# Kernel tuning notes

Hardware: AMD Instinct MI355X
Metric: run time of the kernel (lower is better)

Reference implementation:

```python
import jax, jax.numpy as jnp
import numpy as np
import math

B, T, C, H = 4, 2048, 512, 8
HD = C // H


def make_alibias(block_size, ms):
    # ALiBi-style per-head bias: -m_h * |i - j|, shape [1, H, S, S]
    idx = jnp.arange(block_size)
    dist = jnp.abs(idx[:, None] - idx[None, :]).astype(jnp.float32)  # [S,S]
    return -ms[None, :, None, None] * dist[None, None, :, :]


def setup_inputs() -> dict:
    key = jax.random.key(0)
    k1, k2, k3, k4, k5 = jax.random.split(key, 5)
    x = jax.random.normal(k1, (B, T, C), dtype=jnp.float32)
    Wqkv = jax.random.normal(k2, (C, 3 * C), dtype=jnp.float32) * (1.0 / math.sqrt(C))
    bqkv = jax.random.normal(k3, (3 * C,), dtype=jnp.float32) * 0.02
    Wproj = jax.random.normal(k4, (C, C), dtype=jnp.float32) * (1.0 / math.sqrt(C))
    bproj = jax.random.normal(k5, (C,), dtype=jnp.float32) * 0.02
    ms = jnp.arange(1, H + 1, dtype=jnp.float32) * 0.05
    alibias = make_alibias(T, ms)  # [1,H,T,T]
    return {"x": x, "Wqkv": Wqkv, "bqkv": bqkv, "Wproj": Wproj, "bproj": bproj, "alibias": alibias}


def reference(x, Wqkv, bqkv, Wproj, bproj, alibias):
    Bv, Tv, Cv = x.shape
    qkv = x @ Wqkv + bqkv                      # [B,T,3C]
    q, k, v = jnp.split(qkv, 3, axis=-1)
    # [B,T,C] -> [B,H,T,hd]
    def heads(t):
        return t.reshape(Bv, Tv, H, HD).transpose(0, 2, 1, 3)
    q, k, v = heads(q), heads(k), heads(v)
    att = jnp.einsum('bhqd,bhkd->bhqk', q, k) * (1.0 / math.sqrt(HD))
    att = att + alibias[:, :, :Tv, :Tv]
    att = jax.nn.softmax(att, axis=-1)
    y = jnp.einsum('bhqk,bhkd->bhqd', att, v)  # [B,H,T,hd]
    y = y.transpose(0, 2, 1, 3).reshape(Bv, Tv, Cv)
    return y @ Wproj + bproj
```

## Files before the change

### kernel.cpp

```cpp
#include <hip/hip_runtime.h>
#include <hip/hip_bf16.h>

#define LOG2E 1.4426950408889634f

typedef __attribute__((ext_vector_type(8))) short short8;
typedef __attribute__((ext_vector_type(8))) __bf16 bf16x8;
typedef __attribute__((ext_vector_type(4))) float f32x4;

__device__ __forceinline__ unsigned short f2b(float f){
  unsigned int u = __builtin_bit_cast(unsigned int, f);
  u += 0x7fffu + ((u >> 16) & 1u);
  return (unsigned short)(u >> 16);
}

__device__ __forceinline__ unsigned int cvtpk(float lo, float hi){
  unsigned int r;
  asm("v_cvt_pk_bf16_f32 %0, %1, %2" : "=v"(r) : "v"(lo), "v"(hi));
  return r;
}

__device__ __forceinline__ void gload16(const void* g, void* l){
  __builtin_amdgcn_global_load_lds(
      (const __attribute__((address_space(1))) unsigned int*)g,
      (__attribute__((address_space(3))) unsigned int*)l, 16, 0, 0);
}

__global__ __launch_bounds__(256) void prep_kernel(
    const float* __restrict__ x, const float* __restrict__ Wqkv, const float* __restrict__ Wproj,
    unsigned short* __restrict__ xb, unsigned short* __restrict__ wqkvT, unsigned short* __restrict__ wprojT){
  __shared__ unsigned short T[64][72];
  const int bid = blockIdx.x, tid = threadIdx.x;
  if (bid < 2048){
    size_t i = ((size_t)bid * 256 + tid) * 8;
    float4 a = *(const float4*)(x + i);
    float4 b = *(const float4*)(x + i + 4);
    short8 s;
    s[0]=(short)f2b(a.x); s[1]=(short)f2b(a.y); s[2]=(short)f2b(a.z); s[3]=(short)f2b(a.w);
    s[4]=(short)f2b(b.x); s[5]=(short)f2b(b.y); s[6]=(short)f2b(b.z); s[7]=(short)f2b(b.w);
    *(short8*)(xb + i) = s;
    return;
  }
  const float* in; unsigned short* out; int R, C, bx, by;
  if (bid < 2240){ int t = bid - 2048; bx = t % 24; by = t / 24; in = Wqkv; out = wqkvT; R = 512; C = 1536; }
  else           { int t = bid - 2240; bx = t % 8;  by = t / 8;  in = Wproj; out = wprojT; R = 512; C = 512; }
  const int r0 = by * 64, c0 = bx * 64;
  {
    const int i = tid >> 2, jg = (tid & 3) * 16;
    const float* src = in + (size_t)(r0 + i) * C + c0 + jg;
    #pragma unroll
    for (int e = 0; e < 16; e += 4){
      float4 v = *(const float4*)(src + e);
      T[i][jg + e + 0] = f2b(v.x);
      T[i][jg + e + 1] = f2b(v.y);
      T[i][jg + e + 2] = f2b(v.z);
      T[i][jg + e + 3] = f2b(v.w);
    }
  }
  __syncthreads();
  {
    const int j = tid >> 2, ig = (tid & 3) * 16;
    short8 w0, w1;
    #pragma unroll
    for (int e = 0; e < 8; e++) w0[e] = (short)T[ig + e][j];
    #pragma unroll
    for (int e = 0; e < 8; e++) w1[e] = (short)T[ig + 8 + e][j];
    unsigned short* dst = out + (size_t)(c0 + j) * R + r0 + ig;
    *(short8*)dst = w0;
    *(short8*)(dst + 8) = w1;
  }
}

__global__ __launch_bounds__(256,3) void gemm_qkv_kernel(
    const unsigned short* __restrict__ A,
    const unsigned short* __restrict__ Bt,
    const float* __restrict__ bias,
    unsigned short* __restrict__ Qb,
    unsigned short* __restrict__ Kb,
    unsigned short* __restrict__ VTb,
    float* __restrict__ Mq, float* __restrict__ Mk){
  __shared__ unsigned short As[128*64];
  __shared__ unsigned short Bs[128*64];
  const int tid = threadIdx.x, wid = tid >> 6, lane = tid & 63;
  const int wr = wid >> 1, wc = wid & 1;
  const int fr = lane & 15, fq = lane >> 4;
  const int fr7 = fr & 7;
  const int orig = blockIdx.x;
  const int xcd = orig & 7, idx = orig >> 3;
  const int bm = (xcd + 8*(idx/12)) * 128;
  const int bn = (idx % 12) * 128;
  f32x4 acc[4][4];
  #pragma unroll
  for (int m=0;m<4;m++)
    #pragma unroll
    for (int n=0;n<4;n++) acc[m][n] = (f32x4){0.f,0.f,0.f,0.f};

  for (int k0 = 0; k0 < 512; k0 += 64){
    __syncthreads();
    #pragma unroll
    for (int it=0; it<4; it++){
      const int s = it*256 + tid;
      const int row = s >> 3, c = s & 7;
      const int sc = c ^ (row & 7);
      void* al = (void*)(As + (it*256 + wid*64)*8);
      void* bl = (void*)(Bs + (it*256 + wid*64)*8);
      gload16(A  + (size_t)(bm + row)*512 + k0 + sc*8, al);
      gload16(Bt + (size_t)(bn + row)*512 + k0 + sc*8, bl);
    }
    __syncthreads();
    bf16x8 af[4][2], bfv[4][2];
    #pragma unroll
    for (int m=0;m<4;m++)
      #pragma unroll
      for (int kk=0;kk<2;kk++)
        af[m][kk]  = *(const bf16x8*)&As[(wr*64 + m*16 + fr)*64 + (((kk*4+fq)^fr7)*8)];
    #pragma unroll
    for (int n=0;n<4;n++)
      #pragma unroll
      for (int kk=0;kk<2;kk++)
        bfv[n][kk] = *(const bf16x8*)&Bs[(wc*64 + n*16 + fr)*64 + (((kk*4+fq)^fr7)*8)];
    #pragma unroll
    for (int kk=0;kk<2;kk++)
      #pragma unroll
      for (int m=0;m<4;m++)
        #pragma unroll
        for (int n=0;n<4;n++)
          acc[m][n] = __builtin_amdgcn_mfma_f32_16x16x32_bf16(af[m][kk], bfv[n][kk], acc[m][n], 0,0,0);
  }

  const float SCQ = 0.125f * LOG2E;
  const int colbase = bn + wc*64;
  const int which = colbase >> 9;
  float ss[4][4];
  #pragma unroll
  for (int m=0;m<4;m++)
    #pragma unroll
    for (int g=0;g<4;g++) ss[m][g] = 0.f;

  #pragma unroll
  for (int m=0;m<4;m++){
    const int row0 = bm + wr*64 + m*16 + fq*4;
    const int b_ = row0 >> 11, t_ = row0 & 2047;
    #pragma unroll
    for (int n=0;n<4;n++){
      const int col = colbase + n*16 + fr;
      const int c = col & 511, hh = c >> 6, dd = c & 63;
      const float bv = bias[col];
      if (which == 0){
        #pragma unroll
        for (int g=0; g<4; g++){
          const float v = (acc[m][n][g] + bv) * SCQ;
          ss[m][g] = fmaf(v, v, ss[m][g]);
          Qb[((size_t)(b_*8 + hh)*2048 + t_ + g)*64 + dd] = f2b(v);
        }
      } else if (which == 1){
        #pragma unroll
        for (int g=0; g<4; g++){
          const float v = acc[m][n][g] + bv;
          ss[m][g] = fmaf(v, v, ss[m][g]);
          Kb[((size_t)(b_*8 + hh)*2048 + t_ + g)*64 + dd] = f2b(v);
        }
      } else {
        uint2 pk;
        pk.x = cvtpk(acc[m][n][0] + bv, acc[m][n][1] + bv);
        pk.y = cvtpk(acc[m][n][2] + bv, acc[m][n][3] + bv);
        *(uint2*)&VTb[((size_t)(b_*8 + hh)*64 + dd)*2048 + t_] = pk;
      }
    }
  }

  if (which <= 1){
    #pragma unroll
    for (int m=0;m<4;m++)
      #pragma unroll
      for (int g=0;g<4;g++){
        float s = ss[m][g];
        s += __shfl_xor(s, 1); s += __shfl_xor(s, 2);
        s += __shfl_xor(s, 4); s += __shfl_xor(s, 8);
        ss[m][g] = s;
      }
    float mx = 0.f;
    #pragma unroll
    for (int m=0;m<4;m++)
      #pragma unroll
      for (int g=0;g<4;g++) mx = fmaxf(mx, ss[m][g]);
    mx = fmaxf(mx, __shfl_xor(mx, 16));
    mx = fmaxf(mx, __shfl_xor(mx, 32));
    if (lane == 0){
      const int rowbase = bm + wr*64;
      const int b_ = rowbase >> 11, qc_ = (rowbase >> 6) & 31;
      const int h_ = (colbase >> 6) & 7;
      float* M = which ? Mk : Mq;
      M[(b_*8 + h_)*32 + qc_] = sqrtf(mx) * 1.01f;
    }
  }
}

__global__ __launch_bounds__(256,3) void attn_kernel(
    const unsigned short* __restrict__ Q,
    const unsigned short* __restrict__ K,
    const unsigned short* __restrict__ VT,
    const float* __restrict__ alib,
    const float* __restrict__ Mqa,
    const float* __restrict__ Mka,
    unsigned short* __restrict__ Y){
  __shared__ unsigned short Ks[2][64*64];
  __shared__ unsigned short Vs[2][64*64];
  __shared__ unsigned short Ps[4][16][72];
  __shared__ float MkS[32];
  __shared__ float wred[4];
  __shared__ int lst[32];
  __shared__ int nsh;
  const int tid = threadIdx.x, wid = tid >> 6, lane = tid & 63;
  const int fr = lane & 15, fq = lane >> 4;
  const int fr7 = fr & 7;
  const int id = blockIdx.x;
  const int h = id >> 7;
  const int low3 = id & 7, idx4 = (id & 127) >> 3;
  const int b = idx4 >> 2, off = idx4 & 3;
  const int quad = (low3 - b) & 7;
  const int qc = quad*4 + off;
  const int bh = b*8 + h;
  const int q0 = qc*64 + wid*16;
  const unsigned short* Qp = Q  + (size_t)bh * 131072;
  const unsigned short* Kp = K  + (size_t)bh * 131072;
  const unsigned short* Vp = VT + (size_t)bh * 131072;
  const float nmh2 = alib[(size_t)h * 4194304 + 1] * LOG2E;
  const float MqMk0 = Mqa[bh*32 + qc];
  if (tid < 32) MkS[tid] = Mka[bh*32 + tid];

  float vmk = Mka[bh*32 + (lane & 31)];
  #pragma unroll
  for (int d=1; d<32; d<<=1) vmk = fmaxf(vmk, __shfl_xor(vmk, d));
  const float msta = MqMk0 * vmk;

  bf16x8 qf[2];
  #pragma unroll
  for (int kk=0;kk<2;kk++)
    qf[kk] = *(const bf16x8*)(Qp + (size_t)(q0 + fr)*64 + kk*32 + fq*8);

  bf16x8 ones;
  #pragma unroll
  for (int e=0;e<8;e++) ones[e] = __builtin_bit_cast(__bf16, (unsigned short)0x3F80);

  f32x4 o[4], osum;
  #pragma unroll
  for (int ni=0;ni<4;ni++) o[ni] = (f32x4){0.f,0.f,0.f,0.f};
  osum = (f32x4){0.f,0.f,0.f,0.f};
  float rowmax = -1e30f;
  const float qi = (float)(q0 + fr);
  const float qb = nmh2 * qi;
  f32x4 ka[4];
  #pragma unroll
  for (int ni=0;ni<4;ni++)
    #pragma unroll
    for (int g=0;g<4;g++) ka[ni][g] = nmh2 * (float)(ni*16 + fq*4 + g);

  auto stage = [&](int kt, int buf){
    const int kb = kt * 64;
    #pragma unroll
    for (int it=0; it<2; it++){
      const int s = it*256 + tid;
      const int row = s >> 3, c = s & 7;
      const int sc = c ^ (row & 7);
      gload16(Kp + (size_t)(kb + row)*64 + sc*8, (void*)(Ks[buf] + (it*256 + wid*64)*8));
      gload16(Vp + (size_t)row*2048 + kb + sc*8, (void*)(Vs[buf] + (it*256 + wid*64)*8));
    }
  };

  auto compute = [&](int kt, int buf, bool diag){
    const int kb = kt * 64;
    const unsigned short* KsB = Ks[buf];
    const unsigned short* VsB = Vs[buf];
    bf16x8 kf[4][2], vf[4][2];
    #pragma unroll
    for (int ni=0;ni<4;ni++)
      #pragma unroll
      for (int kk=0;kk<2;kk++){
        const int r = ni*16 + fr;
        const int sw = ((kk*4 + fq) ^ fr7) * 8;
        kf[ni][kk] = *(const bf16x8*)&KsB[r*64 + sw];
        vf[ni][kk] = *(const bf16x8*)&VsB[r*64 + sw];
      }

    f32x4 st[4];
    const f32x4 fz = {0.f,0.f,0.f,0.f};
    #pragma unroll
    for (int ni=0;ni<4;ni++){
      f32x4 t0 = __builtin_amdgcn_mfma_f32_16x16x32_bf16(kf[ni][0], qf[0], fz, 0,0,0);
      st[ni] = __builtin_amdgcn_mfma_f32_16x16x32_bf16(kf[ni][1], qf[1], t0, 0,0,0);
    }

    float cadd;
    if (diag){
      const float base = qi - (float)(kb + fq*4);
      #pragma unroll
      for (int ni=0;ni<4;ni++)
        #pragma unroll
        for (int g=0;g<4;g++){
          const float d = fabsf(base - (float)(ni*16 + g));
          st[ni][g] = fmaf(nmh2, d, st[ni][g]);
        }
      cadd = 0.f;
      float m0 = fmaxf(fmaxf(st[0][0], st[0][1]), fmaxf(st[0][2], st[0][3]));
      float m1 = fmaxf(fmaxf(st[1][0], st[1][1]), fmaxf(st[1][2], st[1][3]));
      float m2 = fmaxf(fmaxf(st[2][0], st[2][1]), fmaxf(st[2][2], st[2][3]));
      float m3 = fmaxf(fmaxf(st[3][0], st[3][1]), fmaxf(st[3][2], st[3][3]));
      float tm = fmaxf(fmaxf(m0, m1), fmaxf(m2, m3));
      tm = fmaxf(tm, __shfl_xor(tm, 16));
      tm = fmaxf(tm, __shfl_xor(tm, 32));
      rowmax = tm;
    } else {
      const float s1 = (kt > qc) ? 1.f : -1.f;
      #pragma unroll
      for (int ni=0;ni<4;ni++)
        #pragma unroll
        for (int g=0;g<4;g++)
          st[ni][g] = fmaf(s1, ka[ni][g], st[ni][g]);
      cadd = s1 * (nmh2 * (float)kb - qb);
    }

    const float mexp = msta - cadd;
    #pragma unroll
    for (int ni=0;ni<4;ni++)
      #pragma unroll
      for (int g=0;g<4;g++)
        st[ni][g] = exp2f(st[ni][g] - mexp);

    #pragma unroll
    for (int ni=0;ni<4;ni++){
      uint2 pk;
      pk.x = cvtpk(st[ni][0], st[ni][1]);
      pk.y = cvtpk(st[ni][2], st[ni][3]);
      *(uint2*)&Ps[wid][fr][ni*16 + fq*4] = pk;
    }

    bf16x8 pf[2];
    #pragma unroll
    for (int kk=0;kk<2;kk++)
      pf[kk] = *(const bf16x8*)&Ps[wid][fr][kk*32 + fq*8];
    #pragma unroll
    for (int ni=0;ni<4;ni++){
      o[ni] = __builtin_amdgcn_mfma_f32_16x16x32_bf16(pf[0], vf[ni][0], o[ni], 0,0,0);
      o[ni] = __builtin_amdgcn_mfma_f32_16x16x32_bf16(pf[1], vf[ni][1], o[ni], 0,0,0);
    }
    osum = __builtin_amdgcn_mfma_f32_16x16x32_bf16(pf[0], ones, osum, 0,0,0);
    osum = __builtin_amdgcn_mfma_f32_16x16x32_bf16(pf[1], ones, osum, 0,0,0);
  };

  const int e0 = (qc + 1 < 32) ? qc + 1 : qc - 1;
  const int e1 = (qc + 1 < 32 && qc - 1 >= 0) ? qc - 1 : -1;
  stage(qc, 0);
  stage(e0, 1);
  asm volatile("s_waitcnt vmcnt(4)" ::: "memory");
  __builtin_amdgcn_sched_barrier(0);
  __builtin_amdgcn_s_barrier();
  compute(qc, 0, true);

  float wm = rowmax;
  #pragma unroll
  for (int d=1; d<16; d<<=1) wm = fminf(wm, __shfl_xor(wm, d));
  if (lane == 0) wred[wid] = wm;
  __syncthreads();
  const float thresh  = fminf(fminf(wred[0], wred[1]), fminf(wred[2], wred[3])) - 14.0f;
  const float threshW = wm - 14.0f;

  if (tid == 0){
    float maxMk = 0.f;
    #pragma unroll
    for (int t=0; t<32; t++) maxMk = fmaxf(maxMk, MkS[t]);
    int n = 0;
    if (e1 >= 0) lst[n++] = e1;
    for (int dt = 2; dt < 32; dt++){
      const float biasmax = nmh2 * (float)((dt - 1)*64 + 1);
      if (MqMk0 * maxMk + biasmax < thresh) break;
      int kt = qc + dt;
      if (kt < 32 && MqMk0 * MkS[kt] + biasmax >= thresh) lst[n++] = kt;
      kt = qc - dt;
      if (kt >= 0 && MqMk0 * MkS[kt] + biasmax >= thresh) lst[n++] = kt;
    }
    nsh = n;
  }
  __syncthreads();
  const int nt = nsh + 1;

  for (int j = 0; j < nt; j++){
    const int kt = (j == 0) ? e0 : lst[j-1];
    asm volatile("s_waitcnt lgkmcnt(0)" ::: "memory");
    __builtin_amdgcn_sched_barrier(0);
    __builtin_amdgcn_s_barrier();
    if (j + 1 < nt){
      stage((j == 0) ? lst[0] : lst[j], j & 1);
      asm volatile("s_waitcnt vmcnt(4)" ::: "memory");
    } else {
      asm volatile("s_waitcnt vmcnt(0)" ::: "memory");
    }
    __builtin_amdgcn_sched_barrier(0);
    __builtin_amdgcn_s_barrier();
    const int dminW = (kt > qc) ? (kt*64 - (q0 + 15)) : (q0 - (kt*64 + 63));
    if (MqMk0 * MkS[kt] + nmh2 * (float)dminW >= threshW)
      compute(kt, (j+1)&1, false);
  }

  #pragma unroll
  for (int g=0;g<4;g++){
    const float iv = 1.0f / osum[g];
    const int t = q0 + fq*4 + g;
    #pragma unroll
    for (int ni=0;ni<4;ni++)
      Y[(size_t)(b*2048 + t)*512 + h*64 + ni*16 + fr] = f2b(o[ni][g] * iv);
  }
}

__global__ __launch_bounds__(256,2) void gemm_proj_kernel(
    const unsigned short* __restrict__ A,
    const unsigned short* __restrict__ Bt,
    const float* __restrict__ bias,
    float* __restrict__ out){
  __shared__ unsigned short As[128*64];
  __shared__ unsigned short Bs[128*64];
  const int tid = threadIdx.x, wid = tid >> 6, lane = tid & 63;
  const int wr = wid >> 1, wc = wid & 1;
  const int fr = lane & 15, fq = lane >> 4;
  const int fr7 = fr & 7;
  const int orig = blockIdx.x;
  const int xcd = orig & 7, idx = orig >> 3;
  const int bm = (xcd + 8*(idx >> 2)) * 128;
  const int bn = (idx & 3) * 128;
  f32x4 acc[4][4];
  #pragma unroll
  for (int m=0;m<4;m++)
    #pragma unroll
    for (int n=0;n<4;n++) acc[m][n] = (f32x4){0.f,0.f,0.f,0.f};

  for (int k0 = 0; k0 < 512; k0 += 64){
    __syncthreads();
    #pragma unroll
    for (int it=0; it<4; it++){
      const int s = it*256 + tid;
      const int row = s >> 3, c = s & 7;
      const int sc = c ^ (row & 7);
      void* al = (void*)(As + (it*256 + wid*64)*8);
      void* bl = (void*)(Bs + (it*256 + wid*64)*8);
      gload16(A  + (size_t)(bm + row)*512 + k0 + sc*8, al);
      gload16(Bt + (size_t)(bn + row)*512 + k0 + sc*8, bl);
    }
    __syncthreads();
    bf16x8 af[4][2], bfv[4][2];
    #pragma unroll
    for (int m=0;m<4;m++)
      #pragma unroll
      for (int kk=0;kk<2;kk++)
        af[m][kk]  = *(const bf16x8*)&As[(wr*64 + m*16 + fr)*64 + (((kk*4+fq)^fr7)*8)];
    #pragma unroll
    for (int n=0;n<4;n++)
      #pragma unroll
      for (int kk=0;kk<2;kk++)
        bfv[n][kk] = *(const bf16x8*)&Bs[(wc*64 + n*16 + fr)*64 + (((kk*4+fq)^fr7)*8)];
    #pragma unroll
    for (int kk=0;kk<2;kk++)
      #pragma unroll
      for (int m=0;m<4;m++)
        #pragma unroll
        for (int n=0;n<4;n++)
          acc[m][n] = __builtin_amdgcn_mfma_f32_16x16x32_bf16(af[m][kk], bfv[n][kk], acc[m][n], 0,0,0);
  }

  #pragma unroll
  for (int m=0;m<4;m++){
    const int row0 = bm + wr*64 + m*16 + fq*4;
    #pragma unroll
    for (int n=0;n<4;n++){
      const int col = bn + wc*64 + n*16 + fr;
      const float bv = bias[col];
      #pragma unroll
      for (int g=0; g<4; g++)
        out[(size_t)(row0 + g)*512 + col] = acc[m][n][g] + bv;
    }
  }
}

extern "C" void kernel_launch(void* const* d_in, const int* in_sizes, int n_in,
                              void* d_out, int out_size, void* d_ws, size_t ws_size,
                              hipStream_t stream){
  const float* x     = (const float*)d_in[0];
  const float* Wqkv  = (const float*)d_in[1];
  const float* bqkv  = (const float*)d_in[2];
  const float* Wproj = (const float*)d_in[3];
  const float* bproj = (const float*)d_in[4];
  const float* alib  = (const float*)d_in[5];
  char* ws = (char*)d_ws;
  unsigned short* xb     = (unsigned short*)(ws);
  unsigned short* wqkvT  = (unsigned short*)(ws + 8388608);
  unsigned short* wprojT = (unsigned short*)(ws + 9961472);
  unsigned short* Qb     = (unsigned short*)(ws + 10485760);
  unsigned short* Kb     = (unsigned short*)(ws + 18874368);
  unsigned short* VTb    = (unsigned short*)(ws + 27262976);
  unsigned short* Yb     = (unsigned short*)(ws + 35651584);
  float* out = (float*)d_out;
  float* Mq = out + 4194304 - 2048;
  float* Mk = Mq + 1024;

  prep_kernel<<<2304, 256, 0, stream>>>(x, Wqkv, Wproj, xb, wqkvT, wprojT);
  gemm_qkv_kernel<<<768, 256, 0, stream>>>(xb, wqkvT, bqkv, Qb, Kb, VTb, Mq, Mk);
  attn_kernel<<<1024, 256, 0, stream>>>(Qb, Kb, VTb, alib, Mq, Mk, Yb);
  gemm_proj_kernel<<<256, 256, 0, stream>>>(Yb, wprojT, bproj, out);
}
```

Baseline: 65.29 us.

## Process two adjacent query chunks per attention block to reuse staged K/V tiles

Each attention block now handles 128 query rows (two 64-row chunks A and B) instead of 64, and the grid is halved to 512 blocks. Each K/V tile staged into LDS is used for both query chunks, with separate per-chunk skip tests, so global K/V loads per query row drop roughly by half. The cost is more registers for the second accumulator set, which may hurt occupancy under the 3-blocks launch bound. There are also fewer blocks in flight and a more serialized start, since both diagonal tiles are processed before the tile list is built.

```diff
diff --git a/kernel.cpp b/kernel.cpp
--- a/kernel.cpp
+++ b/kernel.cpp
@@ -207,48 +207,53 @@
   __shared__ unsigned short Vs[2][64*64];
   __shared__ unsigned short Ps[4][16][72];
   __shared__ float MkS[32];
-  __shared__ float wred[4];
+  __shared__ float wredA[4], wredB[4];
   __shared__ int lst[32];
   __shared__ int nsh;
   const int tid = threadIdx.x, wid = tid >> 6, lane = tid & 63;
   const int fr = lane & 15, fq = lane >> 4;
   const int fr7 = fr & 7;
   const int id = blockIdx.x;
-  const int h = id >> 7;
-  const int low3 = id & 7, idx4 = (id & 127) >> 3;
-  const int b = idx4 >> 2, off = idx4 & 3;
-  const int quad = (low3 - b) & 7;
-  const int qc = quad*4 + off;
+  const int h = id >> 6;
+  const int r_ = id & 63, xcd = r_ & 7, s_ = r_ >> 3;
+  const int b = s_ >> 1;
+  const int c = ((xcd + b) & 7)*2 + (s_ & 1);
   const int bh = b*8 + h;
-  const int q0 = qc*64 + wid*16;
+  const int qcA = 2*c, qcB = qcA + 1;
+  const int q0a = c*128 + wid*16, q0b = q0a + 64;
   const unsigned short* Qp = Q  + (size_t)bh * 131072;
   const unsigned short* Kp = K  + (size_t)bh * 131072;
   const unsigned short* Vp = VT + (size_t)bh * 131072;
   const float nmh2 = alib[(size_t)h * 4194304 + 1] * LOG2E;
-  const float MqMk0 = Mqa[bh*32 + qc];
+  const float MqA = Mqa[bh*32 + qcA];
+  const float MqB = Mqa[bh*32 + qcB];
   if (tid < 32) MkS[tid] = Mka[bh*32 + tid];
 
   float vmk = Mka[bh*32 + (lane & 31)];
   #pragma unroll
   for (int d=1; d<32; d<<=1) vmk = fmaxf(vmk, __shfl_xor(vmk, d));
-  const float msta = MqMk0 * vmk;
-
-  bf16x8 qf[2];
-  #pragma unroll
-  for (int kk=0;kk<2;kk++)
-    qf[kk] = *(const bf16x8*)(Qp + (size_t)(q0 + fr)*64 + kk*32 + fq*8);
+  const float mstaA = MqA * vmk;
+  const float mstaB = MqB * vmk;
+
+  bf16x8 qfA[2], qfB[2];
+  #pragma unroll
+  for (int kk=0;kk<2;kk++){
+    qfA[kk] = *(const bf16x8*)(Qp + (size_t)(q0a + fr)*64 + kk*32 + fq*8);
+    qfB[kk] = *(const bf16x8*)(Qp + (size_t)(q0b + fr)*64 + kk*32 + fq*8);
+  }
 
   bf16x8 ones;
   #pragma unroll
   for (int e=0;e<8;e++) ones[e] = __builtin_bit_cast(__bf16, (unsigned short)0x3F80);
 
-  f32x4 o[4], osum;
-  #pragma unroll
-  for (int ni=0;ni<4;ni++) o[ni] = (f32x4){0.f,0.f,0.f,0.f};
-  osum = (f32x4){0.f,0.f,0.f,0.f};
-  float rowmax = -1e30f;
-  const float qi = (float)(q0 + fr);
-  const float qb = nmh2 * qi;
+  f32x4 oA[4], oB[4], osumA, osumB;
+  #pragma unroll
+  for (int ni=0;ni<4;ni++){ oA[ni] = (f32x4){0.f,0.f,0.f,0.f}; oB[ni] = (f32x4){0.f,0.f,0.f,0.f}; }
+  osumA = (f32x4){0.f,0.f,0.f,0.f};
+  osumB = (f32x4){0.f,0.f,0.f,0.f};
+  float rowmaxA = -1e30f, rowmaxB = -1e30f;
+  const float qiA = (float)(q0a + fr), qiB = (float)(q0b + fr);
+  const float qbA = nmh2 * qiA, qbB = nmh2 * qiB;
   f32x4 ka[4];
   #pragma unroll
   for (int ni=0;ni<4;ni++)
@@ -260,14 +265,14 @@
     #pragma unroll
     for (int it=0; it<2; it++){
       const int s = it*256 + tid;
-      const int row = s >> 3, c = s & 7;
-      const int sc = c ^ (row & 7);
+      const int row = s >> 3, cc = s & 7;
+      const int sc = cc ^ (row & 7);
       gload16(Kp + (size_t)(kb + row)*64 + sc*8, (void*)(Ks[buf] + (it*256 + wid*64)*8));
       gload16(Vp + (size_t)row*2048 + kb + sc*8, (void*)(Vs[buf] + (it*256 + wid*64)*8));
     }
   };
 
-  auto compute = [&](int kt, int buf, bool diag){
+  auto computeT = [&](int kt, int buf, int diagmi, bool doA, bool doB){
     const int kb = kt * 64;
     const unsigned short* KsB = Ks[buf];
     const unsigned short* VsB = Vs[buf];
@@ -281,102 +286,122 @@
         kf[ni][kk] = *(const bf16x8*)&KsB[r*64 + sw];
         vf[ni][kk] = *(const bf16x8*)&VsB[r*64 + sw];
       }
-
-    f32x4 st[4];
     const f32x4 fz = {0.f,0.f,0.f,0.f};
-    #pragma unroll
-    for (int ni=0;ni<4;ni++){
-      f32x4 t0 = __builtin_amdgcn_mfma_f32_16x16x32_bf16(kf[ni][0], qf[0], fz, 0,0,0);
-      st[ni] = __builtin_amdgcn_mfma_f32_16x16x32_bf16(kf[ni][1], qf[1], t0, 0,0,0);
-    }
-
-    float cadd;
-    if (diag){
-      const float base = qi - (float)(kb + fq*4);
+
+    #pragma unroll
+    for (int mi=0; mi<2; mi++){
+      if (mi == 0 ? !doA : !doB) continue;
+      const bf16x8* qf = (mi == 0) ? qfA : qfB;
+      f32x4 st[4];
+      #pragma unroll
+      for (int ni=0;ni<4;ni++){
+        f32x4 t0 = __builtin_amdgcn_mfma_f32_16x16x32_bf16(kf[ni][0], qf[0], fz, 0,0,0);
+        st[ni] = __builtin_amdgcn_mfma_f32_16x16x32_bf16(kf[ni][1], qf[1], t0, 0,0,0);
+      }
+      const float qi_ = (mi==0) ? qiA : qiB;
+      const float qb_ = (mi==0) ? qbA : qbB;
+      const int   qc_ = (mi==0) ? qcA : qcB;
+      float cadd;
+      if (diagmi == mi){
+        const float base = qi_ - (float)(kb + fq*4);
+        #pragma unroll
+        for (int ni=0;ni<4;ni++)
+          #pragma unroll
+          for (int g=0;g<4;g++){
+            const float d = fabsf(base - (float)(ni*16 + g));
+            st[ni][g] = fmaf(nmh2, d, st[ni][g]);
+          }
+        cadd = 0.f;
+        float m0 = fmaxf(fmaxf(st[0][0], st[0][1]), fmaxf(st[0][2], st[0][3]));
+        float m1 = fmaxf(fmaxf(st[1][0], st[1][1]), fmaxf(st[1][2], st[1][3]));
+        float m2 = fmaxf(fmaxf(st[2][0], st[2][1]), fmaxf(st[2][2], st[2][3]));
+        float m3 = fmaxf(fmaxf(st[3][0], st[3][1]), fmaxf(st[3][2], st[3][3]));
+        float tm = fmaxf(fmaxf(m0, m1), fmaxf(m2, m3));
+        tm = fmaxf(tm, __shfl_xor(tm, 16));
+        tm = fmaxf(tm, __shfl_xor(tm, 32));
+        if (mi == 0) rowmaxA = tm; else rowmaxB = tm;
+      } else {
+        const float s1 = (kt > qc_) ? 1.f : -1.f;
+        #pragma unroll
+        for (int ni=0;ni<4;ni++)
+          #pragma unroll
+          for (int g=0;g<4;g++)
+            st[ni][g] = fmaf(s1, ka[ni][g], st[ni][g]);
+        cadd = s1 * (nmh2 * (float)kb - qb_);
+      }
+
+      const float mexp = ((mi==0) ? mstaA : mstaB) - cadd;
       #pragma unroll
       for (int ni=0;ni<4;ni++)
         #pragma unroll
-        for (int g=0;g<4;g++){
-          const float d = fabsf(base - (float)(ni*16 + g));
-          st[ni][g] = fmaf(nmh2, d, st[ni][g]);
-        }
-      cadd = 0.f;
-      float m0 = fmaxf(fmaxf(st[0][0], st[0][1]), fmaxf(st[0][2], st[0][3]));
-      float m1 = fmaxf(fmaxf(st[1][0], st[1][1]), fmaxf(st[1][2], st[1][3]));
-      float m2 = fmaxf(fmaxf(st[2][0], st[2][1]), fmaxf(st[2][2], st[2][3]));
-      float m3 = fmaxf(fmaxf(st[3][0], st[3][1]), fmaxf(st[3][2], st[3][3]));
-      float tm = fmaxf(fmaxf(m0, m1), fmaxf(m2, m3));
-      tm = fmaxf(tm, __shfl_xor(tm, 16));
-      tm = fmaxf(tm, __shfl_xor(tm, 32));
-      rowmax = tm;
-    } else {
-      const float s1 = (kt > qc) ? 1.f : -1.f;
-      #pragma unroll
-      for (int ni=0;ni<4;ni++)
-        #pragma unroll
         for (int g=0;g<4;g++)
-          st[ni][g] = fmaf(s1, ka[ni][g], st[ni][g]);
-      cadd = s1 * (nmh2 * (float)kb - qb);
-    }
-
-    const float mexp = msta - cadd;
-    #pragma unroll
-    for (int ni=0;ni<4;ni++)
-      #pragma unroll
-      for (int g=0;g<4;g++)
-        st[ni][g] = exp2f(st[ni][g] - mexp);
-
-    #pragma unroll
-    for (int ni=0;ni<4;ni++){
-      uint2 pk;
-      pk.x = cvtpk(st[ni][0], st[ni][1]);
-      pk.y = cvtpk(st[ni][2], st[ni][3]);
-      *(uint2*)&Ps[wid][fr][ni*16 + fq*4] = pk;
-    }
-
-    bf16x8 pf[2];
-    #pragma unroll
-    for (int kk=0;kk<2;kk++)
-      pf[kk] = *(const bf16x8*)&Ps[wid][fr][kk*32 + fq*8];
-    #pragma unroll
-    for (int ni=0;ni<4;ni++){
-      o[ni] = __builtin_amdgcn_mfma_f32_16x16x32_bf16(pf[0], vf[ni][0], o[ni], 0,0,0);
-      o[ni] = __builtin_amdgcn_mfma_f32_16x16x32_bf16(pf[1], vf[ni][1], o[ni], 0,0,0);
-    }
-    osum = __builtin_amdgcn_mfma_f32_16x16x32_bf16(pf[0], ones, osum, 0,0,0);
-    osum = __builtin_amdgcn_mfma_f32_16x16x32_bf16(pf[1], ones, osum, 0,0,0);
+          st[ni][g] = exp2f(st[ni][g] - mexp);
+
+      #pragma unroll
+      for (int ni=0;ni<4;ni++){
+        uint2 pk;
+        pk.x = cvtpk(st[ni][0], st[ni][1]);
+        pk.y = cvtpk(st[ni][2], st[ni][3]);
+        *(uint2*)&Ps[wid][fr][ni*16 + fq*4] = pk;
+      }
+      bf16x8 pf[2];
+      #pragma unroll
+      for (int kk=0;kk<2;kk++)
+        pf[kk] = *(const bf16x8*)&Ps[wid][fr][kk*32 + fq*8];
+      f32x4* o_ = (mi==0) ? oA : oB;
+      #pragma unroll
+      for (int ni=0;ni<4;ni++){
+        o_[ni] = __builtin_amdgcn_mfma_f32_16x16x32_bf16(pf[0], vf[ni][0], o_[ni], 0,0,0);
+        o_[ni] = __builtin_amdgcn_mfma_f32_16x16x32_bf16(pf[1], vf[ni][1], o_[ni], 0,0,0);
+      }
+      if (mi == 0){
+        osumA = __builtin_amdgcn_mfma_f32_16x16x32_bf16(pf[0], ones, osumA, 0,0,0);
+        osumA = __builtin_amdgcn_mfma_f32_16x16x32_bf16(pf[1], ones, osumA, 0,0,0);
+      } else {
+        osumB = __builtin_amdgcn_mfma_f32_16x16x32_bf16(pf[0], ones, osumB, 0,0,0);
+        osumB = __builtin_amdgcn_mfma_f32_16x16x32_bf16(pf[1], ones, osumB, 0,0,0);
+      }
+    }
   };
 
-  const int e0 = (qc + 1 < 32) ? qc + 1 : qc - 1;
-  const int e1 = (qc + 1 < 32 && qc - 1 >= 0) ? qc - 1 : -1;
-  stage(qc, 0);
-  stage(e0, 1);
+  stage(qcA, 0);
+  stage(qcB, 1);
   asm volatile("s_waitcnt vmcnt(4)" ::: "memory");
   __builtin_amdgcn_sched_barrier(0);
   __builtin_amdgcn_s_barrier();
-  compute(qc, 0, true);
-
-  float wm = rowmax;
-  #pragma unroll
-  for (int d=1; d<16; d<<=1) wm = fminf(wm, __shfl_xor(wm, d));
-  if (lane == 0) wred[wid] = wm;
+  computeT(qcA, 0, 0, true, true);
+  asm volatile("s_waitcnt vmcnt(0)" ::: "memory");
+  __builtin_amdgcn_sched_barrier(0);
+  __builtin_amdgcn_s_barrier();
+  const int f0 = (qcA - 1 >= 0) ? qcA - 1 : qcB + 1;
+  stage(f0, 0);
+  computeT(qcB, 1, 1, true, true);
+
+  float wmA = rowmaxA, wmB = rowmaxB;
+  #pragma unroll
+  for (int d=1; d<16; d<<=1){ wmA = fminf(wmA, __shfl_xor(wmA, d)); wmB = fminf(wmB, __shfl_xor(wmB, d)); }
+  if (lane == 0){ wredA[wid] = wmA; wredB[wid] = wmB; }
   __syncthreads();
-  const float thresh  = fminf(fminf(wred[0], wred[1]), fminf(wred[2], wred[3])) - 14.0f;
-  const float threshW = wm - 14.0f;
+  const float thresh = fminf(fminf(fminf(wredA[0], wredA[1]), fminf(wredA[2], wredA[3])),
+                             fminf(fminf(wredB[0], wredB[1]), fminf(wredB[2], wredB[3]))) - 14.0f;
+  const float threshWA = wmA - 14.0f;
+  const float threshWB = wmB - 14.0f;
 
   if (tid == 0){
     float maxMk = 0.f;
     #pragma unroll
     for (int t=0; t<32; t++) maxMk = fmaxf(maxMk, MkS[t]);
+    const float Mqmax = fmaxf(MqA, MqB);
     int n = 0;
-    if (e1 >= 0) lst[n++] = e1;
+    if (qcA - 1 >= 0 && qcB + 1 < 32)
+      lst[n++] = (f0 == qcA - 1) ? qcB + 1 : qcA - 1;
     for (int dt = 2; dt < 32; dt++){
       const float biasmax = nmh2 * (float)((dt - 1)*64 + 1);
-      if (MqMk0 * maxMk + biasmax < thresh) break;
-      int kt = qc + dt;
-      if (kt < 32 && MqMk0 * MkS[kt] + biasmax >= thresh) lst[n++] = kt;
-      kt = qc - dt;
-      if (kt >= 0 && MqMk0 * MkS[kt] + biasmax >= thresh) lst[n++] = kt;
+      if (Mqmax * maxMk + biasmax < thresh) break;
+      int kt = qcB + dt;
+      if (kt < 32 && MqB * MkS[kt] + biasmax >= thresh) lst[n++] = kt;
+      kt = qcA - dt;
+      if (kt >= 0 && MqA * MkS[kt] + biasmax >= thresh) lst[n++] = kt;
     }
     nsh = n;
   }
@@ -384,30 +409,36 @@
   const int nt = nsh + 1;
 
   for (int j = 0; j < nt; j++){
-    const int kt = (j == 0) ? e0 : lst[j-1];
+    const int kt = (j == 0) ? f0 : lst[j-1];
     asm volatile("s_waitcnt lgkmcnt(0)" ::: "memory");
     __builtin_amdgcn_sched_barrier(0);
     __builtin_amdgcn_s_barrier();
     if (j + 1 < nt){
-      stage((j == 0) ? lst[0] : lst[j], j & 1);
+      stage(lst[j], (j+1)&1);
       asm volatile("s_waitcnt vmcnt(4)" ::: "memory");
     } else {
       asm volatile("s_waitcnt vmcnt(0)" ::: "memory");
     }
     __builtin_amdgcn_sched_barrier(0);
     __builtin_amdgcn_s_barrier();
-    const int dminW = (kt > qc) ? (kt*64 - (q0 + 15)) : (q0 - (kt*64 + 63));
-    if (MqMk0 * MkS[kt] + nmh2 * (float)dminW >= threshW)
-      compute(kt, (j+1)&1, false);
+    const int dA = (kt > qcB) ? (kt*64 - (q0a + 15)) : (q0a - (kt*64 + 63));
+    const int dB = (kt > qcB) ? (kt*64 - (q0b + 15)) : (q0b - (kt*64 + 63));
+    const bool doA = MqA * MkS[kt] + nmh2 * (float)dA >= threshWA;
+    const bool doB = MqB * MkS[kt] + nmh2 * (float)dB >= threshWB;
+    if (doA || doB) computeT(kt, j&1, -1, doA, doB);
   }
 
   #pragma unroll
   for (int g=0;g<4;g++){
-    const float iv = 1.0f / osum[g];
-    const int t = q0 + fq*4 + g;
-    #pragma unroll
-    for (int ni=0;ni<4;ni++)
-      Y[(size_t)(b*2048 + t)*512 + h*64 + ni*16 + fr] = f2b(o[ni][g] * iv);
+    const float ivA = 1.0f / osumA[g];
+    const float ivB = 1.0f / osumB[g];
+    const int tA = q0a + fq*4 + g;
+    const int tB = q0b + fq*4 + g;
+    #pragma unroll
+    for (int ni=0;ni<4;ni++){
+      Y[(size_t)(b*2048 + tA)*512 + h*64 + ni*16 + fr] = f2b(oA[ni][g] * ivA);
+      Y[(size_t)(b*2048 + tB)*512 + h*64 + ni*16 + fr] = f2b(oB[ni][g] * ivB);
+    }
   }
 }
 
@@ -502,6 +533,6 @@
 
   prep_kernel<<<2304, 256, 0, stream>>>(x, Wqkv, Wproj, xb, wqkvT, wprojT);
   gemm_qkv_kernel<<<768, 256, 0, stream>>>(xb, wqkvT, bqkv, Qb, Kb, VTb, Mq, Mk);
-  attn_kernel<<<1024, 256, 0, stream>>>(Qb, Kb, VTb, alib, Mq, Mk, Yb);
+  attn_kernel<<<512, 256, 0, stream>>>(Qb, Kb, VTb, alib, Mq, Mk, Yb);
   gemm_proj_kernel<<<256, 256, 0, stream>>>(Yb, wprojT, bproj, out);
 }
```

After: 92.20 us. +41.2%, slower.

## Process 128 query rows per attention block with 8 waves sharing K/V tiles

Applied to the files above, without the earlier changes.

The attention kernel now launches 512 blocks of 512 threads, and each block covers two adjacent 64-row query chunks instead of one. Each staged K/V tile in LDS is reused by twice as many waves, which halves the tile loads per query row. Both diagonal tiles are computed with row-max tracking, and the far-tile list is built from the union of the two chunks' bias bounds. The cost is a looser per-block skip threshold, which can add tiles the narrower blocks skipped, plus heavier barriers across 8 waves.

```diff
diff --git a/kernel.cpp b/kernel.cpp
--- a/kernel.cpp
+++ b/kernel.cpp
@@ -195,7 +195,7 @@
   }
 }
 
-__global__ __launch_bounds__(256,3) void attn_kernel(
+__global__ __launch_bounds__(512,4) void attn_kernel(
     const unsigned short* __restrict__ Q,
     const unsigned short* __restrict__ K,
     const unsigned short* __restrict__ VT,
@@ -205,33 +205,34 @@
     unsigned short* __restrict__ Y){
   __shared__ unsigned short Ks[2][64*64];
   __shared__ unsigned short Vs[2][64*64];
-  __shared__ unsigned short Ps[4][16][72];
+  __shared__ unsigned short Ps[8][16][72];
   __shared__ float MkS[32];
-  __shared__ float wred[4];
+  __shared__ float wred[8];
   __shared__ int lst[32];
   __shared__ int nsh;
   const int tid = threadIdx.x, wid = tid >> 6, lane = tid & 63;
   const int fr = lane & 15, fq = lane >> 4;
   const int fr7 = fr & 7;
   const int id = blockIdx.x;
-  const int h = id >> 7;
-  const int low3 = id & 7, idx4 = (id & 127) >> 3;
-  const int b = idx4 >> 2, off = idx4 & 3;
-  const int quad = (low3 - b) & 7;
-  const int qc = quad*4 + off;
+  const int h = id >> 6;
+  const int r_ = id & 63, xcd = r_ & 7, s_ = r_ >> 3;
+  const int b = s_ >> 1;
+  const int c = ((xcd + b) & 7)*2 + (s_ & 1);
   const int bh = b*8 + h;
-  const int q0 = qc*64 + wid*16;
+  const int tA = 2*c, tB = 2*c + 1;
+  const int q0 = c*128 + wid*16;
+  const int qcW = q0 >> 6;
   const unsigned short* Qp = Q  + (size_t)bh * 131072;
   const unsigned short* Kp = K  + (size_t)bh * 131072;
   const unsigned short* Vp = VT + (size_t)bh * 131072;
   const float nmh2 = alib[(size_t)h * 4194304 + 1] * LOG2E;
-  const float MqMk0 = Mqa[bh*32 + qc];
+  const float MqW = Mqa[bh*32 + qcW];
   if (tid < 32) MkS[tid] = Mka[bh*32 + tid];
 
   float vmk = Mka[bh*32 + (lane & 31)];
   #pragma unroll
   for (int d=1; d<32; d<<=1) vmk = fmaxf(vmk, __shfl_xor(vmk, d));
-  const float msta = MqMk0 * vmk;
+  const float msta = MqW * vmk;
 
   bf16x8 qf[2];
   #pragma unroll
@@ -257,17 +258,13 @@
 
   auto stage = [&](int kt, int buf){
     const int kb = kt * 64;
-    #pragma unroll
-    for (int it=0; it<2; it++){
-      const int s = it*256 + tid;
-      const int row = s >> 3, c = s & 7;
-      const int sc = c ^ (row & 7);
-      gload16(Kp + (size_t)(kb + row)*64 + sc*8, (void*)(Ks[buf] + (it*256 + wid*64)*8));
-      gload16(Vp + (size_t)row*2048 + kb + sc*8, (void*)(Vs[buf] + (it*256 + wid*64)*8));
-    }
+    const int row = tid >> 3, cc = tid & 7;
+    const int sc = cc ^ (row & 7);
+    gload16(Kp + (size_t)(kb + row)*64 + sc*8, (void*)(Ks[buf] + wid*64*8));
+    gload16(Vp + (size_t)row*2048 + kb + sc*8, (void*)(Vs[buf] + wid*64*8));
   };
 
-  auto compute = [&](int kt, int buf, bool diag){
+  auto computeT = [&](int kt, int buf, bool track){
     const int kb = kt * 64;
     const unsigned short* KsB = Ks[buf];
     const unsigned short* VsB = Vs[buf];
@@ -291,7 +288,7 @@
     }
 
     float cadd;
-    if (diag){
+    if (kt == qcW){
       const float base = qi - (float)(kb + fq*4);
       #pragma unroll
       for (int ni=0;ni<4;ni++)
@@ -301,6 +298,17 @@
           st[ni][g] = fmaf(nmh2, d, st[ni][g]);
         }
       cadd = 0.f;
+    } else {
+      const float s1 = (kt > qcW) ? 1.f : -1.f;
+      #pragma unroll
+      for (int ni=0;ni<4;ni++)
+        #pragma unroll
+        for (int g=0;g<4;g++)
+          st[ni][g] = fmaf(s1, ka[ni][g], st[ni][g]);
+      cadd = s1 * (nmh2 * (float)kb - qb);
+    }
+
+    if (track){
       float m0 = fmaxf(fmaxf(st[0][0], st[0][1]), fmaxf(st[0][2], st[0][3]));
       float m1 = fmaxf(fmaxf(st[1][0], st[1][1]), fmaxf(st[1][2], st[1][3]));
       float m2 = fmaxf(fmaxf(st[2][0], st[2][1]), fmaxf(st[2][2], st[2][3]));
@@ -308,15 +316,7 @@
       float tm = fmaxf(fmaxf(m0, m1), fmaxf(m2, m3));
       tm = fmaxf(tm, __shfl_xor(tm, 16));
       tm = fmaxf(tm, __shfl_xor(tm, 32));
-      rowmax = tm;
-    } else {
-      const float s1 = (kt > qc) ? 1.f : -1.f;
-      #pragma unroll
-      for (int ni=0;ni<4;ni++)
-        #pragma unroll
-        for (int g=0;g<4;g++)
-          st[ni][g] = fmaf(s1, ka[ni][g], st[ni][g]);
-      cadd = s1 * (nmh2 * (float)kb - qb);
+      rowmax = fmaxf(rowmax, tm + cadd);
     }
 
     const float mexp = msta - cadd;
@@ -347,36 +347,46 @@
     osum = __builtin_amdgcn_mfma_f32_16x16x32_bf16(pf[1], ones, osum, 0,0,0);
   };
 
-  const int e0 = (qc + 1 < 32) ? qc + 1 : qc - 1;
-  const int e1 = (qc + 1 < 32 && qc - 1 >= 0) ? qc - 1 : -1;
-  stage(qc, 0);
-  stage(e0, 1);
-  asm volatile("s_waitcnt vmcnt(4)" ::: "memory");
+  const int f0 = (tA - 1 >= 0) ? tA - 1 : tB + 1;
+  stage(tA, 0);
+  stage(tB, 1);
+  asm volatile("s_waitcnt vmcnt(2)" ::: "memory");
   __builtin_amdgcn_sched_barrier(0);
   __builtin_amdgcn_s_barrier();
-  compute(qc, 0, true);
+  computeT(tA, 0, true);
+  asm volatile("s_waitcnt vmcnt(0)" ::: "memory");
+  __builtin_amdgcn_sched_barrier(0);
+  __builtin_amdgcn_s_barrier();
+  stage(f0, 0);
+  computeT(tB, 1, true);
 
   float wm = rowmax;
   #pragma unroll
   for (int d=1; d<16; d<<=1) wm = fminf(wm, __shfl_xor(wm, d));
   if (lane == 0) wred[wid] = wm;
   __syncthreads();
-  const float thresh  = fminf(fminf(wred[0], wred[1]), fminf(wred[2], wred[3])) - 14.0f;
+  float thresh = wred[0];
+  #pragma unroll
+  for (int w=1; w<8; w++) thresh = fminf(thresh, wred[w]);
+  thresh -= 14.0f;
   const float threshW = wm - 14.0f;
 
   if (tid == 0){
     float maxMk = 0.f;
     #pragma unroll
     for (int t=0; t<32; t++) maxMk = fmaxf(maxMk, MkS[t]);
+    const float MqA = Mqa[bh*32 + tA];
+    const float MqB = Mqa[bh*32 + tB];
+    const float Mqmax = fmaxf(MqA, MqB);
     int n = 0;
-    if (e1 >= 0) lst[n++] = e1;
+    if (tA - 1 >= 0 && tB + 1 < 32) lst[n++] = tB + 1;
     for (int dt = 2; dt < 32; dt++){
       const float biasmax = nmh2 * (float)((dt - 1)*64 + 1);
-      if (MqMk0 * maxMk + biasmax < thresh) break;
-      int kt = qc + dt;
-      if (kt < 32 && MqMk0 * MkS[kt] + biasmax >= thresh) lst[n++] = kt;
-      kt = qc - dt;
-      if (kt >= 0 && MqMk0 * MkS[kt] + biasmax >= thresh) lst[n++] = kt;
+      if (Mqmax * maxMk + biasmax < thresh) break;
+      int kt = tB + dt;
+      if (kt < 32 && MqB * MkS[kt] + biasmax >= thresh) lst[n++] = kt;
+      kt = tA - dt;
+      if (kt >= 0 && MqA * MkS[kt] + biasmax >= thresh) lst[n++] = kt;
     }
     nsh = n;
   }
@@ -384,21 +394,21 @@
   const int nt = nsh + 1;
 
   for (int j = 0; j < nt; j++){
-    const int kt = (j == 0) ? e0 : lst[j-1];
+    const int kt = (j == 0) ? f0 : lst[j-1];
     asm volatile("s_waitcnt lgkmcnt(0)" ::: "memory");
     __builtin_amdgcn_sched_barrier(0);
     __builtin_amdgcn_s_barrier();
     if (j + 1 < nt){
-      stage((j == 0) ? lst[0] : lst[j], j & 1);
-      asm volatile("s_waitcnt vmcnt(4)" ::: "memory");
+      stage(lst[j], (j+1)&1);
+      asm volatile("s_waitcnt vmcnt(2)" ::: "memory");
     } else {
       asm volatile("s_waitcnt vmcnt(0)" ::: "memory");
     }
     __builtin_amdgcn_sched_barrier(0);
     __builtin_amdgcn_s_barrier();
-    const int dminW = (kt > qc) ? (kt*64 - (q0 + 15)) : (q0 - (kt*64 + 63));
-    if (MqMk0 * MkS[kt] + nmh2 * (float)dminW >= threshW)
-      compute(kt, (j+1)&1, false);
+    const int dminW = (kt*64 > q0 + 15) ? (kt*64 - (q0 + 15)) : (q0 - (kt*64 + 63));
+    if (MqW * MkS[kt] + nmh2 * (float)dminW >= threshW)
+      computeT(kt, j&1, false);
   }
 
   #pragma unroll
@@ -502,6 +512,6 @@
 
   prep_kernel<<<2304, 256, 0, stream>>>(x, Wqkv, Wproj, xb, wqkvT, wprojT);
   gemm_qkv_kernel<<<768, 256, 0, stream>>>(xb, wqkvT, bqkv, Qb, Kb, VTb, Mq, Mk);
-  attn_kernel<<<1024, 256, 0, stream>>>(Qb, Kb, VTb, alib, Mq, Mk, Yb);
+  attn_kernel<<<512, 512, 0, stream>>>(Qb, Kb, VTb, alib, Mq, Mk, Yb);
   gemm_proj_kernel<<<256, 256, 0, stream>>>(Yb, wprojT, bproj, out);
 }
```

Result: slower. 82.69 us (+26.6%).
